# Optimization experiments

Hardware: AMD Instinct MI355X
Metric: run time of the kernel (lower is better)

Reference implementation:

```python
import jax, jax.numpy as jnp
import numpy as np

N = 50000        # nodes
E = 800000       # edges (avg degree 16)
NODE_D = 128     # node_attr_dim
EDGE_D = 16      # edge_attr_dim
HID = 300        # hidden_dim (module default)


def setup_inputs() -> dict:
    key = jax.random.key(0)
    ks = jax.random.split(key, 8)
    x = jax.random.normal(ks[0], (N, NODE_D), jnp.float32)
    edge_attr = jax.random.normal(ks[1], (E, EDGE_D), jnp.float32)
    edge_weight = jax.random.uniform(ks[2], (E,), jnp.float32)
    node_weight = jax.random.uniform(ks[3], (N,), jnp.float32)
    edge_index = jax.random.randint(ks[4], (2, E), 0, N, jnp.int32)
    # lin0: Linear(node_attr_dim + edge_attr_dim, hidden_dim)
    W0 = jax.random.normal(ks[5], (NODE_D + EDGE_D, HID), jnp.float32) / np.sqrt(NODE_D + EDGE_D)
    b0 = jnp.zeros((HID,), jnp.float32)
    # mp_layer.linear: Linear(hidden_dim, hidden_dim)
    W = jax.random.normal(ks[6], (HID, HID), jnp.float32) / np.sqrt(HID)
    b = jnp.zeros((HID,), jnp.float32)
    return dict(x=x, edge_attr=edge_attr, edge_weight=edge_weight,
                node_weight=node_weight, W0=W0, b0=b0, W=W, b=b,
                edge_index=edge_index)


def reference(x, edge_attr, edge_weight, node_weight, W0, b0, W, b, edge_index):
    src = edge_index[0]   # x_j (source, flow='source_to_target')
    dst = edge_index[1]   # aggregation target i
    n = x.shape[0]

    # --- isFirstLayer: weighted sum of incoming edge features, scattered at dst ---
    inc = jax.ops.segment_sum(edge_weight[:, None] * edge_attr, dst, num_segments=n)  # [N, EDGE_D]
    h0 = jax.nn.relu(jnp.concatenate([x, inc], axis=1) @ W0 + b0)                     # [N, HID]

    # --- MessagePassingLayer: message = edge_weight * x_j; aggr = mean at dst ---
    msg = edge_weight[:, None] * h0[src]                                              # [E, HID]
    agg = jax.ops.segment_sum(msg, dst, num_segments=n)                               # [N, HID]
    deg = jax.ops.segment_sum(jnp.ones((src.shape[0],), x.dtype), dst, num_segments=n)
    agg = agg / jnp.maximum(deg, 1.0)[:, None]  # scatter-mean (0 where no incoming edges)

    # --- update: relu(h0 + linear(aggr)) (add_residual=True) ---
    h = jax.nn.relu(h0 + agg @ W + b)
    # isLastLayer=False -> no node_weight scaling
    return (h, h0)
```

## Files before the change

kernel.cpp:

```cpp
#include <hip/hip_runtime.h>

#define NN 50000
#define NE 800000
#define ND 128
#define ED 16
#define HID 300
#define KP1 192
#define KP2 320
#define NP 320

#define SCAN_T 256
#define SCAN_B ((NN + SCAN_T - 1) / SCAN_T)

typedef __attribute__((ext_vector_type(8))) short short8;
typedef __attribute__((ext_vector_type(4))) float f32x4;

__device__ __forceinline__ unsigned short f2b(float f) {
    unsigned int u = __float_as_uint(f);
    u = (u + 0x7FFFu + ((u >> 16) & 1u)) >> 16;
    return (unsigned short)u;
}
__device__ __forceinline__ float blo(unsigned int u) {
    return __uint_as_float(u << 16);
}
__device__ __forceinline__ float bhi(unsigned int u) {
    return __uint_as_float(u & 0xffff0000u);
}

__device__ __forceinline__ int block_iscan(int v, int tid) {
    int lane = tid & 63;
    #pragma unroll
    for (int off = 1; off < 64; off <<= 1) {
        int t = __shfl_up(v, off);
        if (lane >= off) v += t;
    }
    __shared__ int wsum[4];
    int wid = tid >> 6;
    if (lane == 63) wsum[wid] = v;
    __syncthreads();
    int add = 0;
    #pragma unroll
    for (int w = 0; w < 4; ++w)
        if (w < wid) add += wsum[w];
    return v + add;
}

__global__ void hist_kernel(const int* __restrict__ ei, int* __restrict__ rowptr) {
    int e = blockIdx.x * blockDim.x + threadIdx.x;
    if (e < NE) atomicAdd(&rowptr[ei[NE + e] + 1], 1);
}

__global__ __launch_bounds__(SCAN_T) void scan1(int* __restrict__ rowptr,
                                                int* __restrict__ blockSums) {
    int i = blockIdx.x * SCAN_T + threadIdx.x;
    int v = (i < NN) ? rowptr[1 + i] : 0;
    v = block_iscan(v, threadIdx.x);
    if (i < NN) rowptr[1 + i] = v;
    if (threadIdx.x == SCAN_T - 1) blockSums[blockIdx.x] = v;
}

__global__ __launch_bounds__(SCAN_T) void scan2(int* __restrict__ blockSums) {
    int t = threadIdx.x;
    int orig = (t < SCAN_B) ? blockSums[t] : 0;
    int v = block_iscan(orig, t);
    if (t < SCAN_B) blockSums[t] = v - orig;
}

__global__ __launch_bounds__(SCAN_T) void scan3(int* __restrict__ rowptr,
                                                const int* __restrict__ blockSums,
                                                int* __restrict__ cursor) {
    int i = blockIdx.x * SCAN_T + threadIdx.x;
    if (i < NN) {
        int v = rowptr[1 + i] + blockSums[blockIdx.x];
        rowptr[1 + i] = v;
        if (i + 1 < NN) cursor[i + 1] = v;
    }
    if (i == 0) cursor[0] = 0;
}

__global__ void fill_kernel(const int* __restrict__ ei, const float* __restrict__ ew,
                            int* __restrict__ cursor, int* __restrict__ csr_src,
                            float* __restrict__ csr_w, int* __restrict__ csr_eid) {
    int e = blockIdx.x * blockDim.x + threadIdx.x;
    if (e < NE) {
        int d = ei[NE + e];
        int pos = atomicAdd(&cursor[d], 1);
        csr_src[pos] = ei[e];
        csr_w[pos]   = ew[e];
        csr_eid[pos] = e;
    }
}

__global__ __launch_bounds__(256) void cast_x(const float* __restrict__ x,
                                              unsigned short* __restrict__ A1) {
    int tid = blockIdx.x * blockDim.x + threadIdx.x;
    if (tid >= NN * 32) return;
    int n = tid >> 5, q = tid & 31;
    float4 v = *(const float4*)&x[(size_t)n * ND + q * 4];
    unsigned short o[4] = {f2b(v.x), f2b(v.y), f2b(v.z), f2b(v.w)};
    *(uint2*)&A1[(size_t)n * KP1 + q * 4] = *(uint2*)o;
}

__global__ __launch_bounds__(256) void inc_kernel(
    const float* __restrict__ edge_attr,
    const int* __restrict__ rowptr,
    const float* __restrict__ csr_w,
    const int* __restrict__ csr_eid,
    unsigned short* __restrict__ A1) {
    int n = (blockIdx.x * blockDim.x + threadIdx.x) >> 6;
    int lane = threadIdx.x & 63;
    if (n >= NN) return;
    int g = lane >> 4, j = lane & 15;
    int lo = rowptr[n], hi = rowptr[n + 1];
    float v = 0.f;
    for (int k = lo + g; k < hi; k += 4) {
        float w = csr_w[k];
        int eid = csr_eid[k];
        v += w * edge_attr[(size_t)eid * ED + j];
    }
    v += __shfl_xor(v, 16);
    v += __shfl_xor(v, 32);
    if (lane < 16)
        A1[(size_t)n * KP1 + ND + lane] = f2b(v);
    else
        A1[(size_t)n * KP1 + ND + lane] = 0;
}

__global__ void castB0(const float* __restrict__ W0, unsigned short* __restrict__ B0T) {
    int n = blockIdx.x, k = threadIdx.x;
    float v = (n < HID && k < ND + ED) ? W0[(size_t)k * HID + n] : 0.f;
    B0T[(size_t)n * KP1 + k] = f2b(v);
}

__global__ void castB(const float* __restrict__ W, unsigned short* __restrict__ BT) {
    int n = blockIdx.x, k = threadIdx.x;
    float v = (n < HID && k < HID) ? W[(size_t)k * HID + n] : 0.f;
    BT[(size_t)n * KP2 + k] = f2b(v);
}

template <int MODE, int KP>
__global__ __launch_bounds__(256) void gemm_mfma(
    const unsigned short* __restrict__ A,
    const unsigned short* __restrict__ BT,
    const float* __restrict__ bias,
    const float* __restrict__ RES,
    float* __restrict__ C,
    unsigned short* __restrict__ h0b,
    int M)
{
    __shared__ unsigned short As[128][64];
    __shared__ unsigned short Bs[64][64];
    const int tid = threadIdx.x;
    const int m0 = blockIdx.x * 128;
    const int n0 = blockIdx.y * 64;
    const int wave = tid >> 6, lane = tid & 63;
    const int wm = wave >> 1, wn = wave & 1;
    const int quad = lane >> 4, lr = lane & 15;
    f32x4 acc[4][2] = {};

    for (int kb = 0; kb < KP; kb += 64) {
        #pragma unroll
        for (int i = 0; i < 4; ++i) {
            int s = tid + i * 256;
            int r = s >> 3, c = (s & 7) * 8;
            int mg = m0 + r; if (mg >= M) mg = M - 1;
            *(uint4*)&As[r][c] = *(const uint4*)&A[(size_t)mg * KP + kb + c];
        }
        #pragma unroll
        for (int i = 0; i < 2; ++i) {
            int s = tid + i * 256;
            int r = s >> 3, c = (s & 7) * 8;
            *(uint4*)&Bs[r][c] = *(const uint4*)&BT[(size_t)(n0 + r) * KP + kb + c];
        }
        __syncthreads();
        #pragma unroll
        for (int ks = 0; ks < 2; ++ks) {
            short8 a[4], b[2];
            #pragma unroll
            for (int tm = 0; tm < 4; ++tm)
                a[tm] = *(const short8*)&As[wm * 64 + tm * 16 + lr][ks * 32 + quad * 8];
            #pragma unroll
            for (int tn = 0; tn < 2; ++tn)
                b[tn] = *(const short8*)&Bs[wn * 32 + tn * 16 + lr][ks * 32 + quad * 8];
            #pragma unroll
            for (int tm = 0; tm < 4; ++tm)
                #pragma unroll
                for (int tn = 0; tn < 2; ++tn)
                    acc[tm][tn] = __builtin_amdgcn_mfma_f32_16x16x32_bf16(
                        a[tm], b[tn], acc[tm][tn], 0, 0, 0);
        }
        __syncthreads();
    }
    #pragma unroll
    for (int tm = 0; tm < 4; ++tm) {
        #pragma unroll
        for (int tn = 0; tn < 2; ++tn) {
            int ng = n0 + wn * 32 + tn * 16 + lr;
            #pragma unroll
            for (int r = 0; r < 4; ++r) {
                int mg = m0 + wm * 64 + tm * 16 + quad * 4 + r;
                if (mg < M && ng < HID) {
                    float v = acc[tm][tn][r] + bias[ng];
                    if (MODE == 1) v += RES[(size_t)mg * HID + ng];
                    v = fmaxf(v, 0.f);
                    C[(size_t)mg * HID + ng] = v;
                    if (MODE == 0) h0b[(size_t)mg * NP + ng] = f2b(v);
                }
            }
        }
    }
}

__global__ __launch_bounds__(256) void agg_kernel(
    const unsigned short* __restrict__ h0b,
    const int* __restrict__ rowptr,
    const int* __restrict__ csr_src,
    const float* __restrict__ csr_w,
    unsigned short* __restrict__ aggB)
{
    int n = (blockIdx.x * blockDim.x + threadIdx.x) >> 6;
    int lane = threadIdx.x & 63;
    if (n >= NN) return;
    int lo = rowptr[n], hi = rowptr[n + 1];
    float acc[8] = {};
    const uint4* h4 = (const uint4*)h0b;
    bool act = lane < 40;
    int k = lo;
    for (; k + 1 < hi; k += 2) {
        int s0 = csr_src[k], s1 = csr_src[k + 1];
        float w0 = csr_w[k], w1 = csr_w[k + 1];
        uint4 r0 = {0, 0, 0, 0}, r1 = {0, 0, 0, 0};
        if (act) {
            r0 = h4[(size_t)s0 * 40 + lane];
            r1 = h4[(size_t)s1 * 40 + lane];
        }
        acc[0] += w0 * blo(r0.x); acc[1] += w0 * bhi(r0.x);
        acc[2] += w0 * blo(r0.y); acc[3] += w0 * bhi(r0.y);
        acc[4] += w0 * blo(r0.z); acc[5] += w0 * bhi(r0.z);
        acc[6] += w0 * blo(r0.w); acc[7] += w0 * bhi(r0.w);
        acc[0] += w1 * blo(r1.x); acc[1] += w1 * bhi(r1.x);
        acc[2] += w1 * blo(r1.y); acc[3] += w1 * bhi(r1.y);
        acc[4] += w1 * blo(r1.z); acc[5] += w1 * bhi(r1.z);
        acc[6] += w1 * blo(r1.w); acc[7] += w1 * bhi(r1.w);
    }
    if (k < hi) {
        int s0 = csr_src[k];
        float w0 = csr_w[k];
        uint4 r0 = {0, 0, 0, 0};
        if (act) r0 = h4[(size_t)s0 * 40 + lane];
        acc[0] += w0 * blo(r0.x); acc[1] += w0 * bhi(r0.x);
        acc[2] += w0 * blo(r0.y); acc[3] += w0 * bhi(r0.y);
        acc[4] += w0 * blo(r0.z); acc[5] += w0 * bhi(r0.z);
        acc[6] += w0 * blo(r0.w); acc[7] += w0 * bhi(r0.w);
    }
    if (act) {
        float invd = 1.f / fmaxf((float)(hi - lo), 1.f);
        int cbase = lane * 8;
        unsigned int o[4];
        #pragma unroll
        for (int i = 0; i < 4; ++i) {
            int c0 = cbase + 2 * i, c1 = c0 + 1;
            unsigned int ulo = (c0 < HID) ? f2b(acc[2 * i] * invd) : 0;
            unsigned int uhi = (c1 < HID) ? f2b(acc[2 * i + 1] * invd) : 0;
            o[i] = ulo | (uhi << 16);
        }
        uint4* a4 = (uint4*)aggB;
        uint4 v; v.x = o[0]; v.y = o[1]; v.z = o[2]; v.w = o[3];
        a4[(size_t)n * 40 + lane] = v;
    }
}

extern "C" void kernel_launch(void* const* d_in, const int* in_sizes, int n_in,
                              void* d_out, int out_size, void* d_ws, size_t ws_size,
                              hipStream_t stream) {
    const float* x           = (const float*)d_in[0];
    const float* edge_attr   = (const float*)d_in[1];
    const float* edge_weight = (const float*)d_in[2];
    const float* W0 = (const float*)d_in[4];
    const float* b0 = (const float*)d_in[5];
    const float* W  = (const float*)d_in[6];
    const float* b  = (const float*)d_in[7];
    const int* ei   = (const int*)d_in[8];

    float* out = (float*)d_out;
    float* h  = out;
    float* h0 = out + (size_t)NN * HID;

    char* p = (char*)d_ws;
    auto alloc = [&](size_t bytes) { char* q = p; p += (bytes + 255) & ~(size_t)255; return q; };
    int*   rowptr  = (int*)  alloc((NN + 1) * sizeof(int));
    int*   cursor  = (int*)  alloc(NN * sizeof(int));
    int*   bsums   = (int*)  alloc(SCAN_B * sizeof(int));
    int*   csr_src = (int*)  alloc(NE * sizeof(int));
    float* csr_w   = (float*)alloc(NE * sizeof(float));
    int*   csr_eid = (int*)  alloc(NE * sizeof(int));
    unsigned short* A1   = (unsigned short*)alloc((size_t)NN * KP1 * 2);
    unsigned short* h0b  = (unsigned short*)alloc((size_t)NN * NP * 2);
    unsigned short* aggB = (unsigned short*)alloc((size_t)NN * NP * 2);
    unsigned short* B0T  = (unsigned short*)alloc((size_t)NP * KP1 * 2);
    unsigned short* BT   = (unsigned short*)alloc((size_t)NP * KP2 * 2);

    hipMemsetAsync(rowptr, 0, (NN + 1) * sizeof(int), stream);
    hist_kernel<<<(NE + 255) / 256, 256, 0, stream>>>(ei, rowptr);
    scan1<<<SCAN_B, SCAN_T, 0, stream>>>(rowptr, bsums);
    scan2<<<1, SCAN_T, 0, stream>>>(bsums);
    scan3<<<SCAN_B, SCAN_T, 0, stream>>>(rowptr, bsums, cursor);
    fill_kernel<<<(NE + 255) / 256, 256, 0, stream>>>(ei, edge_weight, cursor,
                                                      csr_src, csr_w, csr_eid);
    castB0<<<NP, KP1, 0, stream>>>(W0, B0T);
    castB<<<NP, KP2, 0, stream>>>(W, BT);
    cast_x<<<(NN * 32 + 255) / 256, 256, 0, stream>>>(x, A1);
    inc_kernel<<<(NN + 3) / 4, 256, 0, stream>>>(edge_attr, rowptr, csr_w,
                                                 csr_eid, A1);

    dim3 g((NN + 127) / 128, NP / 64);
    gemm_mfma<0, KP1><<<g, 256, 0, stream>>>(A1, B0T, b0, nullptr, h0, h0b, NN);
    agg_kernel<<<(NN + 3) / 4, 256, 0, stream>>>(h0b, rowptr, csr_src, csr_w, aggB);
    gemm_mfma<1, KP2><<<g, 256, 0, stream>>>(aggB, BT, b, h0, h, nullptr, NN);
}
```

Baseline: 509.4 us.

## Widen GEMM N-tile to 160, use direct global-to-LDS loads, pack CSR arrays

The GEMM tile grows from 128x64 to 128x160, so each wave computes a 64x80 block and the A tile is re-read by 2 column blocks instead of 5. Tiles are now loaded with global_load_lds builtins, which write straight into LDS and skip the VGPR staging copy. The CSR source/weight and edge-id/weight arrays are packed into interleaved uint2 pairs so each edge costs one 8-byte load in the aggregation and incoming-feature kernels. The trade-off is more accumulator registers and LDS per block, which may lower occupancy, plus fewer blocks in the grid.

```diff
diff --git a/kernel.cpp b/kernel.cpp
--- a/kernel.cpp
+++ b/kernel.cpp
@@ -25,6 +25,12 @@
 }
 __device__ __forceinline__ float bhi(unsigned int u) {
     return __uint_as_float(u & 0xffff0000u);
+}
+
+__device__ __forceinline__ void gload16(const void* g, void* l) {
+    __builtin_amdgcn_global_load_lds(
+        (const __attribute__((address_space(1))) void*)g,
+        (__attribute__((address_space(3))) void*)l, 16, 0, 0);
 }
 
 __device__ __forceinline__ int block_iscan(int v, int tid) {
@@ -79,15 +85,17 @@
 }
 
 __global__ void fill_kernel(const int* __restrict__ ei, const float* __restrict__ ew,
-                            int* __restrict__ cursor, int* __restrict__ csr_src,
-                            float* __restrict__ csr_w, int* __restrict__ csr_eid) {
+                            int* __restrict__ cursor, uint2* __restrict__ csr_sw,
+                            uint2* __restrict__ csr_ew) {
     int e = blockIdx.x * blockDim.x + threadIdx.x;
     if (e < NE) {
         int d = ei[NE + e];
         int pos = atomicAdd(&cursor[d], 1);
-        csr_src[pos] = ei[e];
-        csr_w[pos]   = ew[e];
-        csr_eid[pos] = e;
+        unsigned int wb = __float_as_uint(ew[e]);
+        uint2 sw; sw.x = (unsigned int)ei[e]; sw.y = wb;
+        uint2 ee; ee.x = (unsigned int)e;     ee.y = wb;
+        csr_sw[pos] = sw;
+        csr_ew[pos] = ee;
     }
 }
 
@@ -104,8 +112,7 @@
 __global__ __launch_bounds__(256) void inc_kernel(
     const float* __restrict__ edge_attr,
     const int* __restrict__ rowptr,
-    const float* __restrict__ csr_w,
-    const int* __restrict__ csr_eid,
+    const uint2* __restrict__ csr_ew,
     unsigned short* __restrict__ A1) {
     int n = (blockIdx.x * blockDim.x + threadIdx.x) >> 6;
     int lane = threadIdx.x & 63;
@@ -114,9 +121,9 @@
     int lo = rowptr[n], hi = rowptr[n + 1];
     float v = 0.f;
     for (int k = lo + g; k < hi; k += 4) {
-        float w = csr_w[k];
-        int eid = csr_eid[k];
-        v += w * edge_attr[(size_t)eid * ED + j];
+        uint2 ewp = csr_ew[k];
+        float w = __uint_as_float(ewp.y);
+        v += w * edge_attr[(size_t)ewp.x * ED + j];
     }
     v += __shfl_xor(v, 16);
     v += __shfl_xor(v, 32);
@@ -149,43 +156,43 @@
     int M)
 {
     __shared__ unsigned short As[128][64];
-    __shared__ unsigned short Bs[64][64];
+    __shared__ unsigned short Bs[160][64];
     const int tid = threadIdx.x;
     const int m0 = blockIdx.x * 128;
-    const int n0 = blockIdx.y * 64;
+    const int n0 = blockIdx.y * 160;
     const int wave = tid >> 6, lane = tid & 63;
     const int wm = wave >> 1, wn = wave & 1;
     const int quad = lane >> 4, lr = lane & 15;
-    f32x4 acc[4][2] = {};
+    const int lr8 = lane >> 3;
+    const int lc8 = (lane & 7) * 8;
+    f32x4 acc[4][5] = {};
 
     for (int kb = 0; kb < KP; kb += 64) {
         #pragma unroll
         for (int i = 0; i < 4; ++i) {
-            int s = tid + i * 256;
-            int r = s >> 3, c = (s & 7) * 8;
-            int mg = m0 + r; if (mg >= M) mg = M - 1;
-            *(uint4*)&As[r][c] = *(const uint4*)&A[(size_t)mg * KP + kb + c];
-        }
-        #pragma unroll
-        for (int i = 0; i < 2; ++i) {
-            int s = tid + i * 256;
-            int r = s >> 3, c = (s & 7) * 8;
-            *(uint4*)&Bs[r][c] = *(const uint4*)&BT[(size_t)(n0 + r) * KP + kb + c];
+            int r = wave * 32 + i * 8;
+            int mg = m0 + r + lr8; if (mg >= M) mg = M - 1;
+            gload16(&A[(size_t)mg * KP + kb + lc8], &As[0][0] + r * 64);
+        }
+        #pragma unroll
+        for (int i = 0; i < 5; ++i) {
+            int r = wave * 40 + i * 8;
+            gload16(&BT[(size_t)(n0 + r + lr8) * KP + kb + lc8], &Bs[0][0] + r * 64);
         }
         __syncthreads();
         #pragma unroll
         for (int ks = 0; ks < 2; ++ks) {
-            short8 a[4], b[2];
+            short8 a[4], b[5];
             #pragma unroll
             for (int tm = 0; tm < 4; ++tm)
                 a[tm] = *(const short8*)&As[wm * 64 + tm * 16 + lr][ks * 32 + quad * 8];
             #pragma unroll
-            for (int tn = 0; tn < 2; ++tn)
-                b[tn] = *(const short8*)&Bs[wn * 32 + tn * 16 + lr][ks * 32 + quad * 8];
+            for (int tn = 0; tn < 5; ++tn)
+                b[tn] = *(const short8*)&Bs[wn * 80 + tn * 16 + lr][ks * 32 + quad * 8];
             #pragma unroll
             for (int tm = 0; tm < 4; ++tm)
                 #pragma unroll
-                for (int tn = 0; tn < 2; ++tn)
+                for (int tn = 0; tn < 5; ++tn)
                     acc[tm][tn] = __builtin_amdgcn_mfma_f32_16x16x32_bf16(
                         a[tm], b[tn], acc[tm][tn], 0, 0, 0);
         }
@@ -194,8 +201,8 @@
     #pragma unroll
     for (int tm = 0; tm < 4; ++tm) {
         #pragma unroll
-        for (int tn = 0; tn < 2; ++tn) {
-            int ng = n0 + wn * 32 + tn * 16 + lr;
+        for (int tn = 0; tn < 5; ++tn) {
+            int ng = n0 + wn * 80 + tn * 16 + lr;
             #pragma unroll
             for (int r = 0; r < 4; ++r) {
                 int mg = m0 + wm * 64 + tm * 16 + quad * 4 + r;
@@ -214,8 +221,7 @@
 __global__ __launch_bounds__(256) void agg_kernel(
     const unsigned short* __restrict__ h0b,
     const int* __restrict__ rowptr,
-    const int* __restrict__ csr_src,
-    const float* __restrict__ csr_w,
+    const uint2* __restrict__ csr_sw,
     unsigned short* __restrict__ aggB)
 {
     int n = (blockIdx.x * blockDim.x + threadIdx.x) >> 6;
@@ -227,8 +233,9 @@
     bool act = lane < 40;
     int k = lo;
     for (; k + 1 < hi; k += 2) {
-        int s0 = csr_src[k], s1 = csr_src[k + 1];
-        float w0 = csr_w[k], w1 = csr_w[k + 1];
+        uint2 p0 = csr_sw[k], p1 = csr_sw[k + 1];
+        int s0 = (int)p0.x, s1 = (int)p1.x;
+        float w0 = __uint_as_float(p0.y), w1 = __uint_as_float(p1.y);
         uint4 r0 = {0, 0, 0, 0}, r1 = {0, 0, 0, 0};
         if (act) {
             r0 = h4[(size_t)s0 * 40 + lane];
@@ -244,8 +251,9 @@
         acc[6] += w1 * blo(r1.w); acc[7] += w1 * bhi(r1.w);
     }
     if (k < hi) {
-        int s0 = csr_src[k];
-        float w0 = csr_w[k];
+        uint2 p0 = csr_sw[k];
+        int s0 = (int)p0.x;
+        float w0 = __uint_as_float(p0.y);
         uint4 r0 = {0, 0, 0, 0};
         if (act) r0 = h4[(size_t)s0 * 40 + lane];
         acc[0] += w0 * blo(r0.x); acc[1] += w0 * bhi(r0.x);
@@ -291,9 +299,8 @@
     int*   rowptr  = (int*)  alloc((NN + 1) * sizeof(int));
     int*   cursor  = (int*)  alloc(NN * sizeof(int));
     int*   bsums   = (int*)  alloc(SCAN_B * sizeof(int));
-    int*   csr_src = (int*)  alloc(NE * sizeof(int));
-    float* csr_w   = (float*)alloc(NE * sizeof(float));
-    int*   csr_eid = (int*)  alloc(NE * sizeof(int));
+    uint2* csr_sw  = (uint2*)alloc((size_t)NE * sizeof(uint2));
+    uint2* csr_ew  = (uint2*)alloc((size_t)NE * sizeof(uint2));
     unsigned short* A1   = (unsigned short*)alloc((size_t)NN * KP1 * 2);
     unsigned short* h0b  = (unsigned short*)alloc((size_t)NN * NP * 2);
     unsigned short* aggB = (unsigned short*)alloc((size_t)NN * NP * 2);
@@ -306,15 +313,14 @@
     scan2<<<1, SCAN_T, 0, stream>>>(bsums);
     scan3<<<SCAN_B, SCAN_T, 0, stream>>>(rowptr, bsums, cursor);
     fill_kernel<<<(NE + 255) / 256, 256, 0, stream>>>(ei, edge_weight, cursor,
-                                                      csr_src, csr_w, csr_eid);
+                                                      csr_sw, csr_ew);
     castB0<<<NP, KP1, 0, stream>>>(W0, B0T);
     castB<<<NP, KP2, 0, stream>>>(W, BT);
     cast_x<<<(NN * 32 + 255) / 256, 256, 0, stream>>>(x, A1);
-    inc_kernel<<<(NN + 3) / 4, 256, 0, stream>>>(edge_attr, rowptr, csr_w,
-                                                 csr_eid, A1);
-
-    dim3 g((NN + 127) / 128, NP / 64);
+    inc_kernel<<<(NN + 3) / 4, 256, 0, stream>>>(edge_attr, rowptr, csr_ew, A1);
+
+    dim3 g((NN + 127) / 128, NP / 160);
     gemm_mfma<0, KP1><<<g, 256, 0, stream>>>(A1, B0T, b0, nullptr, h0, h0b, NN);
-    agg_kernel<<<(NN + 3) / 4, 256, 0, stream>>>(h0b, rowptr, csr_src, csr_w, aggB);
+    agg_kernel<<<(NN + 3) / 4, 256, 0, stream>>>(h0b, rowptr, csr_sw, aggB);
     gemm_mfma<1, KP2><<<g, 256, 0, stream>>>(aggB, BT, b, h0, h, nullptr, NN);
 }
```

Measured after the change: 529.3 us. 3.9% more time.
